# Performance work log

Measured on AMD Instinct MI355X. Metric: run time of the kernel, lower is better.

## Reference

```python
import jax, jax.numpy as jnp
import numpy as np

N, K, H = 98, 10, 4        # landmarks, neighbors/node, heads
B, CIN, HC = 1024, 256, 64 # batch, in_channels, head_channels
NEG = -9e15


def setup_inputs() -> dict:
    key = jax.random.key(0)
    ks = jax.random.split(key, 3)
    rng = np.random.default_rng(0)
    # fixed sparsity pattern: K unique neighbors per row, row-major order
    cols2d = np.stack([np.sort(rng.choice(N, K, replace=False)) for _ in range(N)])
    rows = np.repeat(np.arange(N), K)
    cols = cols2d.reshape(-1)
    x = jax.random.normal(ks[0], (B, N, CIN), jnp.float32)
    W = jax.random.normal(ks[1], (H, 2, CIN, HC), jnp.float32) * 0.05  # xavier-ish
    e = jnp.ones((H, N * K), jnp.float32)  # nn.init.constant_(e, 1)
    stdv = 1.0 / np.sqrt(HC)
    bias = jax.random.uniform(ks[2], (H, HC), jnp.float32, -stdv, stdv)
    return {"x": x, "W": W, "e": e, "bias": bias,
            "rows": jnp.asarray(rows, jnp.int32),
            "cols": jnp.asarray(cols, jnp.int32)}


def reference(x, W, e, bias, rows, cols):
    # h0/h1 for all heads at once: [2, H, B, N, HC]
    h = jnp.einsum('bnc,hscd->shbnd', x, W)
    h0, h1 = h[0], h[1]
    # masked adjacency logits per head: -9e15 everywhere, learned e at edges
    base = jnp.full((N, N), NEG, jnp.float32)
    logits = jax.vmap(lambda eh: base.at[rows, cols].set(eh))(e)  # [H,N,N]
    A = jax.nn.softmax(logits, axis=-1)  # F.softmax(adj, dim=1) on [N,N]
    diag = jnp.diagonal(A, axis1=-2, axis2=-1)  # [H,N] -> adj*M part
    A_off = A - diag[..., None] * jnp.eye(N, dtype=A.dtype)  # adj*(1-M)
    out = diag[:, None, :, None] * h0 + jnp.einsum('hij,hbjd->hbid', A_off, h1)
    out = out + bias[:, None, None, :]  # [H,B,N,HC]
    # concat heads along channel dim -> [B, N, H*HC]
    return jnp.transpose(out, (1, 2, 0, 3)).reshape(B, N, H * HC)
```

## Files before the change

kernel.cpp:

```cpp
#include <hip/hip_runtime.h>

typedef __bf16 bf16;
typedef bf16 bf16x4 __attribute__((ext_vector_type(4)));
typedef bf16 bf16x8 __attribute__((ext_vector_type(8)));
typedef float f32x4 __attribute__((ext_vector_type(4)));

#define NND 98
#define KNB 10
#define NH 4
#define CIN 256
#define HC 64
#define CROW_E 132
#define WP_BYTES 262144
#define XA_TILE (7 * 8 * 64 * 8)

__device__ __forceinline__ bf16x8 load_a8(const float* p) {
  f32x4 u = *(const f32x4*)p;
  f32x4 v = *(const f32x4*)(p + 4);
  bf16x8 a;
  a[0] = (bf16)u[0]; a[1] = (bf16)u[1]; a[2] = (bf16)u[2]; a[3] = (bf16)u[3];
  a[4] = (bf16)v[0]; a[5] = (bf16)v[1]; a[6] = (bf16)v[2]; a[7] = (bf16)v[3];
  return a;
}

__global__ __launch_bounds__(256) void prep_kernel(const float* __restrict__ W,
                                                   bf16* __restrict__ Wp,
                                                   const float* __restrict__ x,
                                                   bf16* __restrict__ xa, int B) {
  if (blockIdx.x < 64) {
    int t = blockIdx.x * 256 + threadIdx.x;
    if (t >= 8 * 8 * 4 * 64) return;
    int lane = t & 63;
    int nt = (t >> 6) & 3;
    int kt = (t >> 8) & 7;
    int hs = t >> 11;
    int n = nt * 16 + (lane & 15);
    int kb = kt * 32 + (lane >> 4) * 8;
    const float* src = W + (hs * CIN + kb) * HC + n;
    bf16x8 v;
#pragma unroll
    for (int j = 0; j < 8; ++j) v[j] = (bf16)src[j * HC];
    *(bf16x8*)(Wp + (long long)t * 8) = v;
    return;
  }
  int u = (blockIdx.x - 64) * 256 + threadIdx.x;
  int total = B * 7 * 8 * 64;
  if (u >= total) return;
  int lane = u & 63;
  int kt = (u >> 6) & 7;
  int v = u >> 9;
  int b = v / 7;
  int mt = v - b * 7;
  int row = mt * 16 + (lane & 15);
  int k0 = kt * 32 + (lane >> 4) * 8;
  bf16x8 a = {};
  if (row < NND) a = load_a8(x + ((long long)b * NND + row) * CIN + k0);
  *(bf16x8*)(xa + (long long)u * 8) = a;
}

template <bool XA>
__global__ __launch_bounds__(512, 4) void semgconv_kernel(
    const float* __restrict__ x, const bf16* __restrict__ xa,
    const float* __restrict__ e, const float* __restrict__ bias,
    const int* __restrict__ cols, const bf16* __restrict__ Wp,
    float* __restrict__ out, int nwg) {
  __shared__ __align__(16) bf16 C2[2][112 * CROW_E];
  __shared__ float w_lds[NND * KNB];
  __shared__ short cols_lds[NND * KNB];
  __shared__ float diag_lds[NND];

  const int tid = threadIdx.x;
  int n = blockIdx.x;
  int w = ((nwg & 7) == 0) ? ((n & 7) * (nwg >> 3) + (n >> 3)) : n;
  const int bp = w >> 2;
  const int h = w & 3;
  const int b0 = bp * 2;

  const int lane = tid & 63;
  const int wv = tid >> 6;
  const int wm = wv & 3;
  const int sh = wv >> 2;
  const int mt0 = wm * 2;
  const bool has1 = (mt0 + 1 < 7);

  if (tid < NND) {
    const int i = tid;
    const int* cp = cols + i * KNB;
    const float* ep = e + (h * NND + i) * KNB;
    float ev[KNB];
    int cv[KNB];
    float mx = -3.0e38f;
#pragma unroll
    for (int j = 0; j < KNB; ++j) { cv[j] = cp[j]; ev[j] = ep[j]; mx = fmaxf(mx, ev[j]); }
    float s = 0.f;
#pragma unroll
    for (int j = 0; j < KNB; ++j) { ev[j] = __expf(ev[j] - mx); s += ev[j]; }
    const float inv = 1.f / s;
    float dg = 0.f;
#pragma unroll
    for (int j = 0; j < KNB; ++j) {
      float wj = ev[j] * inv;
      if (cv[j] == i) { dg = wj; wj = 0.f; }
      w_lds[i * KNB + j] = wj;
      cols_lds[i * KNB + j] = (short)cv[j];
    }
    diag_lds[i] = dg;
  }

  f32x4 acc[2][2][4] = {};
  {
    const bf16* wpl = Wp + ((long long)((h * 2 + sh) * 32) * 64 + lane) * 8;
    if (XA) {
      const bf16* ax0 = xa + (((long long)b0 * 7 + mt0) * 8 * 64 + lane) * 8;
      const bf16* ax1 = ax0 + XA_TILE;
#pragma unroll
      for (int kt = 0; kt < 8; ++kt) {
        bf16x8 a00 = *(const bf16x8*)(ax0 + kt * 512);
        bf16x8 a10 = *(const bf16x8*)(ax1 + kt * 512);
        bf16x8 a01 = {}, a11 = {};
        if (has1) {
          a01 = *(const bf16x8*)(ax0 + 4096 + kt * 512);
          a11 = *(const bf16x8*)(ax1 + 4096 + kt * 512);
        }
        bf16x8 bfr[4];
#pragma unroll
        for (int nt = 0; nt < 4; ++nt)
          bfr[nt] = *(const bf16x8*)(wpl + (long long)((kt * 4 + nt) * 64) * 8);
#pragma unroll
        for (int nt = 0; nt < 4; ++nt) {
          acc[0][0][nt] = __builtin_amdgcn_mfma_f32_16x16x32_bf16(a00, bfr[nt], acc[0][0][nt], 0, 0, 0);
          acc[1][0][nt] = __builtin_amdgcn_mfma_f32_16x16x32_bf16(a10, bfr[nt], acc[1][0][nt], 0, 0, 0);
        }
        if (has1) {
#pragma unroll
          for (int nt = 0; nt < 4; ++nt) {
            acc[0][1][nt] = __builtin_amdgcn_mfma_f32_16x16x32_bf16(a01, bfr[nt], acc[0][1][nt], 0, 0, 0);
            acc[1][1][nt] = __builtin_amdgcn_mfma_f32_16x16x32_bf16(a11, bfr[nt], acc[1][1][nt], 0, 0, 0);
          }
        }
      }
    } else {
      const int r0 = mt0 * 16 + (lane & 15);
      const int kb = (lane >> 4) * 8;
      const bool ok0 = (r0 < NND);
#pragma unroll
      for (int kt = 0; kt < 8; ++kt) {
        bf16x8 afr[2][2];
#pragma unroll
        for (int it2 = 0; it2 < 2; ++it2) {
          const float* ap = x + ((long long)(b0 + it2) * NND + r0) * CIN + kb;
          afr[it2][0] = ok0 ? load_a8(ap + kt * 32) : bf16x8{};
          afr[it2][1] = has1 ? load_a8(ap + 16 * CIN + kt * 32) : bf16x8{};
        }
        bf16x8 bfr[4];
#pragma unroll
        for (int nt = 0; nt < 4; ++nt)
          bfr[nt] = *(const bf16x8*)(wpl + (long long)((kt * 4 + nt) * 64) * 8);
#pragma unroll
        for (int it2 = 0; it2 < 2; ++it2)
#pragma unroll
          for (int im = 0; im < 2; ++im)
            if (im == 0 || has1)
#pragma unroll
              for (int nt = 0; nt < 4; ++nt)
                acc[it2][im][nt] = __builtin_amdgcn_mfma_f32_16x16x32_bf16(
                    afr[it2][im], bfr[nt], acc[it2][im][nt], 0, 0, 0);
      }
    }
  }

  {
    const int rowb = mt0 * 16 + (lane >> 4) * 4;
    const int colb = sh * 64 + (lane & 15);
#pragma unroll
    for (int it2 = 0; it2 < 2; ++it2) {
#pragma unroll
      for (int im = 0; im < 2; ++im) {
        if (mt0 + im < 7) {
#pragma unroll
          for (int nt = 0; nt < 4; ++nt) {
            const int col = colb + nt * 16;
#pragma unroll
            for (int r = 0; r < 4; ++r)
              C2[it2][(rowb + im * 16 + r) * CROW_E + col] = (bf16)acc[it2][im][nt][r];
          }
        }
      }
    }
  }
  __syncthreads();

  {
    const int d4 = (tid & 15) * 4;
    const int ig = tid >> 4;
    f32x4 bs = *(const f32x4*)(bias + h * HC + d4);
#pragma unroll
    for (int it2 = 0; it2 < 2; ++it2) {
      const bf16* C = C2[it2];
      float* outb = out + (long long)(b0 + it2) * (NND * NH * HC) + h * HC + d4;
#pragma unroll
      for (int p = 0; p < 4; ++p) {
        const int i = p * 32 + ig;
        if (i < NND) {
          f32x4 av = bs;
          const float dg = diag_lds[i];
          bf16x4 c0 = *(const bf16x4*)(C + i * CROW_E + d4);
          av[0] += dg * (float)c0[0];
          av[1] += dg * (float)c0[1];
          av[2] += dg * (float)c0[2];
          av[3] += dg * (float)c0[3];
#pragma unroll
          for (int j = 0; j < KNB; ++j) {
            const float wj = w_lds[i * KNB + j];
            const int cj = cols_lds[i * KNB + j];
            bf16x4 c1 = *(const bf16x4*)(C + cj * CROW_E + HC + d4);
            av[0] += wj * (float)c1[0];
            av[1] += wj * (float)c1[1];
            av[2] += wj * (float)c1[2];
            av[3] += wj * (float)c1[3];
          }
          *(f32x4*)(outb + (long long)i * (NH * HC)) = av;
        }
      }
    }
  }
}

extern "C" void kernel_launch(void* const* d_in, const int* in_sizes, int n_in,
                              void* d_out, int out_size, void* d_ws, size_t ws_size,
                              hipStream_t stream) {
  const float* x    = (const float*)d_in[0];
  const float* W    = (const float*)d_in[1];
  const float* e    = (const float*)d_in[2];
  const float* bias = (const float*)d_in[3];
  const int* cols   = (const int*)d_in[5];
  float* out        = (float*)d_out;

  int B = in_sizes[0] / (NND * CIN);

  bf16* Wp = (bf16*)d_ws;
  bf16* xa = (bf16*)((char*)d_ws + WP_BYTES);
  const long long xa_bytes = (long long)B * XA_TILE * (long long)sizeof(bf16);
  const bool use_xa = (long long)ws_size >= (long long)WP_BYTES + xa_bytes;

  int xa_blocks = use_xa ? (B * 7 * 8 * 64) / 256 : 0;
  prep_kernel<<<64 + xa_blocks, 256, 0, stream>>>(W, Wp, x, xa, B);

  const int nwg = (B / 2) * NH;
  if (use_xa)
    semgconv_kernel<true><<<nwg, 512, 0, stream>>>(x, xa, e, bias, cols, Wp, out, nwg);
  else
    semgconv_kernel<false><<<nwg, 512, 0, stream>>>(x, xa, e, bias, cols, Wp, out, nwg);
}
```

Before: 240.3 us.

## Replace sparse gather aggregation with dense fp16 MFMA over precomputed adjacency

The per-row sparse gather over 10 neighbors plus diagonal term is replaced by a dense MFMA GEMM. A prep kernel builds a [112x224] fp16 adjacency matrix per head (off-diagonal weights plus diagonal weights in a second block) and packs it into MFMA fragment layout. Each workgroup stores its h0/h1 products transposed in LDS as fp16 and multiplies them against this matrix. The x-to-bf16 packing now goes through a swizzled LDS tile for coalesced access, and the non-workspace fallback path is removed. The trade is more (mostly zero) FLOPs and fp16 intermediate precision in exchange for removing scattered LDS gathers and per-block softmax work.

```diff
diff --git a/kernel.cpp b/kernel.cpp
--- a/kernel.cpp
+++ b/kernel.cpp
@@ -3,6 +3,9 @@
 typedef __bf16 bf16;
 typedef bf16 bf16x4 __attribute__((ext_vector_type(4)));
 typedef bf16 bf16x8 __attribute__((ext_vector_type(8)));
+typedef _Float16 half_t;
+typedef half_t half4 __attribute__((ext_vector_type(4)));
+typedef half_t half8 __attribute__((ext_vector_type(8)));
 typedef float f32x4 __attribute__((ext_vector_type(4)));
 
 #define NND 98
@@ -10,26 +13,25 @@
 #define NH 4
 #define CIN 256
 #define HC 64
-#define CROW_E 132
+#define KAG 224
+#define SROW 232
+#define XA_TILE (7 * 8 * 64 * 8)
+
+#define WP_OFF   0
 #define WP_BYTES 262144
-#define XA_TILE (7 * 8 * 64 * 8)
-
-__device__ __forceinline__ bf16x8 load_a8(const float* p) {
-  f32x4 u = *(const f32x4*)p;
-  f32x4 v = *(const f32x4*)(p + 4);
-  bf16x8 a;
-  a[0] = (bf16)u[0]; a[1] = (bf16)u[1]; a[2] = (bf16)u[2]; a[3] = (bf16)u[3];
-  a[4] = (bf16)v[0]; a[5] = (bf16)v[1]; a[6] = (bf16)v[2]; a[7] = (bf16)v[3];
-  return a;
-}
-
-__global__ __launch_bounds__(256) void prep_kernel(const float* __restrict__ W,
-                                                   bf16* __restrict__ Wp,
-                                                   const float* __restrict__ x,
-                                                   bf16* __restrict__ xa, int B) {
+#define G2D_OFF  (WP_OFF + WP_BYTES)
+#define G2D_BYTES (NH * 112 * KAG * 2)
+#define G2A_OFF  (G2D_OFF + G2D_BYTES)
+#define G2A_BYTES (NH * 49 * 64 * 8 * 2)
+#define XA_OFF   (G2A_OFF + G2A_BYTES)
+
+__global__ __launch_bounds__(256) void misc1_kernel(const float* __restrict__ W,
+                                                    bf16* __restrict__ Wp,
+                                                    const float* __restrict__ e,
+                                                    const int* __restrict__ cols,
+                                                    half_t* __restrict__ G2d) {
   if (blockIdx.x < 64) {
     int t = blockIdx.x * 256 + threadIdx.x;
-    if (t >= 8 * 8 * 4 * 64) return;
     int lane = t & 63;
     int nt = (t >> 6) & 3;
     int kt = (t >> 8) & 7;
@@ -43,184 +45,190 @@
     *(bf16x8*)(Wp + (long long)t * 8) = v;
     return;
   }
-  int u = (blockIdx.x - 64) * 256 + threadIdx.x;
-  int total = B * 7 * 8 * 64;
-  if (u >= total) return;
-  int lane = u & 63;
-  int kt = (u >> 6) & 7;
-  int v = u >> 9;
-  int b = v / 7;
-  int mt = v - b * 7;
-  int row = mt * 16 + (lane & 15);
-  int k0 = kt * 32 + (lane >> 4) * 8;
-  bf16x8 a = {};
-  if (row < NND) a = load_a8(x + ((long long)b * NND + row) * CIN + k0);
-  *(bf16x8*)(xa + (long long)u * 8) = a;
-}
-
-template <bool XA>
+  const int h = blockIdx.x - 64;
+  half_t* g = G2d + h * 112 * KAG;
+  for (int i = threadIdx.x; i < 112 * KAG / 2; i += 256) ((unsigned int*)g)[i] = 0u;
+  __syncthreads();
+  const int i = threadIdx.x;
+  if (i < NND) {
+    const int* cp = cols + i * KNB;
+    const float* ep = e + (h * NND + i) * KNB;
+    float ev[KNB];
+    int cv[KNB];
+    float mx = -3.0e38f;
+#pragma unroll
+    for (int j = 0; j < KNB; ++j) { cv[j] = cp[j]; ev[j] = ep[j]; mx = fmaxf(mx, ev[j]); }
+    float s = 0.f;
+#pragma unroll
+    for (int j = 0; j < KNB; ++j) { ev[j] = __expf(ev[j] - mx); s += ev[j]; }
+    const float inv = 1.f / s;
+    float dg = 0.f;
+#pragma unroll
+    for (int j = 0; j < KNB; ++j) {
+      float wj = ev[j] * inv;
+      if (cv[j] == i) { dg = wj; wj = 0.f; }
+      g[i * KAG + cv[j]] = (half_t)wj;
+    }
+    g[i * KAG + 112 + i] = (half_t)dg;
+  }
+}
+
+__global__ __launch_bounds__(256) void misc2_kernel(const half_t* __restrict__ G2d,
+                                                    half_t* __restrict__ G2a,
+                                                    const float* __restrict__ x,
+                                                    bf16* __restrict__ xa, int B) {
+  if (blockIdx.x < 49) {
+    int t = blockIdx.x * 256 + threadIdx.x;
+    int lane = t & 63;
+    int q = t >> 6;
+    int kt = q % 7;
+    int mt = (q / 7) % 7;
+    int h = q / 49;
+    int row = mt * 16 + (lane & 15);
+    int k0 = kt * 32 + (lane >> 4) * 8;
+    half8 v = *(const half8*)(G2d + (h * 112 + row) * KAG + k0);
+    *(half8*)(G2a + (long long)t * 8) = v;
+    return;
+  }
+  __shared__ __align__(16) bf16 xs[16 * 256];
+  const int b = blockIdx.x - 49;
+  const int tid = threadIdx.x;
+  const float* xb = x + (long long)b * NND * CIN;
+  for (int mt = 0; mt < 7; ++mt) {
+#pragma unroll
+    for (int it = 0; it < 4; ++it) {
+      int chunk = tid + it * 256;
+      int r = chunk >> 6;
+      int c4 = chunk & 63;
+      int g = mt * 16 + r;
+      f32x4 v = {0.f, 0.f, 0.f, 0.f};
+      if (g < NND) v = *(const f32x4*)(xb + g * CIN + c4 * 4);
+      bf16x4 bv;
+      bv[0] = (bf16)v[0]; bv[1] = (bf16)v[1]; bv[2] = (bf16)v[2]; bv[3] = (bf16)v[3];
+      int byte = (r * 512 + c4 * 8) ^ ((r & 7) << 4);
+      *(bf16x4*)((char*)xs + byte) = bv;
+    }
+    __syncthreads();
+#pragma unroll
+    for (int it = 0; it < 2; ++it) {
+      int u = tid + it * 256;
+      int kt = u >> 6;
+      int lane = u & 63;
+      int r = lane & 15;
+      int byte = (r * 512 + kt * 64 + (lane >> 4) * 16) ^ ((r & 7) << 4);
+      bf16x8 f = *(const bf16x8*)((char*)xs + byte);
+      *(bf16x8*)(xa + ((((long long)b * 7 + mt) * 8 + kt) * 64 + lane) * 8) = f;
+    }
+    __syncthreads();
+  }
+}
+
 __global__ __launch_bounds__(512, 4) void semgconv_kernel(
-    const float* __restrict__ x, const bf16* __restrict__ xa,
-    const float* __restrict__ e, const float* __restrict__ bias,
-    const int* __restrict__ cols, const bf16* __restrict__ Wp,
+    const bf16* __restrict__ xa, const half_t* __restrict__ G2a,
+    const bf16* __restrict__ Wp, const float* __restrict__ bias,
     float* __restrict__ out, int nwg) {
-  __shared__ __align__(16) bf16 C2[2][112 * CROW_E];
-  __shared__ float w_lds[NND * KNB];
-  __shared__ short cols_lds[NND * KNB];
-  __shared__ float diag_lds[NND];
+  __shared__ __align__(16) half_t S[2][64 * SROW];
 
   const int tid = threadIdx.x;
+  const int lane = tid & 63;
+  const int wv = tid >> 6;
+
   int n = blockIdx.x;
   int w = ((nwg & 7) == 0) ? ((n & 7) * (nwg >> 3) + (n >> 3)) : n;
   const int bp = w >> 2;
   const int h = w & 3;
   const int b0 = bp * 2;
 
-  const int lane = tid & 63;
-  const int wv = tid >> 6;
   const int wm = wv & 3;
   const int sh = wv >> 2;
   const int mt0 = wm * 2;
   const bool has1 = (mt0 + 1 < 7);
 
-  if (tid < NND) {
-    const int i = tid;
-    const int* cp = cols + i * KNB;
-    const float* ep = e + (h * NND + i) * KNB;
-    float ev[KNB];
-    int cv[KNB];
-    float mx = -3.0e38f;
-#pragma unroll
-    for (int j = 0; j < KNB; ++j) { cv[j] = cp[j]; ev[j] = ep[j]; mx = fmaxf(mx, ev[j]); }
-    float s = 0.f;
-#pragma unroll
-    for (int j = 0; j < KNB; ++j) { ev[j] = __expf(ev[j] - mx); s += ev[j]; }
-    const float inv = 1.f / s;
-    float dg = 0.f;
-#pragma unroll
-    for (int j = 0; j < KNB; ++j) {
-      float wj = ev[j] * inv;
-      if (cv[j] == i) { dg = wj; wj = 0.f; }
-      w_lds[i * KNB + j] = wj;
-      cols_lds[i * KNB + j] = (short)cv[j];
-    }
-    diag_lds[i] = dg;
-  }
-
   f32x4 acc[2][2][4] = {};
   {
     const bf16* wpl = Wp + ((long long)((h * 2 + sh) * 32) * 64 + lane) * 8;
-    if (XA) {
-      const bf16* ax0 = xa + (((long long)b0 * 7 + mt0) * 8 * 64 + lane) * 8;
-      const bf16* ax1 = ax0 + XA_TILE;
-#pragma unroll
-      for (int kt = 0; kt < 8; ++kt) {
-        bf16x8 a00 = *(const bf16x8*)(ax0 + kt * 512);
-        bf16x8 a10 = *(const bf16x8*)(ax1 + kt * 512);
-        bf16x8 a01 = {}, a11 = {};
-        if (has1) {
-          a01 = *(const bf16x8*)(ax0 + 4096 + kt * 512);
-          a11 = *(const bf16x8*)(ax1 + 4096 + kt * 512);
+    const bf16* ax0 = xa + (((long long)b0 * 7 + mt0) * 8 * 64 + lane) * 8;
+    const bf16* ax1 = ax0 + XA_TILE;
+#pragma unroll
+    for (int kt = 0; kt < 8; ++kt) {
+      bf16x8 a00 = *(const bf16x8*)(ax0 + kt * 512);
+      bf16x8 a10 = *(const bf16x8*)(ax1 + kt * 512);
+      bf16x8 a01 = {}, a11 = {};
+      if (has1) {
+        a01 = *(const bf16x8*)(ax0 + 4096 + kt * 512);
+        a11 = *(const bf16x8*)(ax1 + 4096 + kt * 512);
+      }
+      bf16x8 bfr[4];
+#pragma unroll
+      for (int nt = 0; nt < 4; ++nt)
+        bfr[nt] = *(const bf16x8*)(wpl + (long long)((kt * 4 + nt) * 64) * 8);
+#pragma unroll
+      for (int nt = 0; nt < 4; ++nt) {
+        acc[0][0][nt] = __builtin_amdgcn_mfma_f32_16x16x32_bf16(a00, bfr[nt], acc[0][0][nt], 0, 0, 0);
+        acc[1][0][nt] = __builtin_amdgcn_mfma_f32_16x16x32_bf16(a10, bfr[nt], acc[1][0][nt], 0, 0, 0);
+      }
+      if (has1) {
+#pragma unroll
+        for (int nt = 0; nt < 4; ++nt) {
+          acc[0][1][nt] = __builtin_amdgcn_mfma_f32_16x16x32_bf16(a01, bfr[nt], acc[0][1][nt], 0, 0, 0);
+          acc[1][1][nt] = __builtin_amdgcn_mfma_f32_16x16x32_bf16(a11, bfr[nt], acc[1][1][nt], 0, 0, 0);
         }
-        bf16x8 bfr[4];
-#pragma unroll
-        for (int nt = 0; nt < 4; ++nt)
-          bfr[nt] = *(const bf16x8*)(wpl + (long long)((kt * 4 + nt) * 64) * 8);
-#pragma unroll
-        for (int nt = 0; nt < 4; ++nt) {
-          acc[0][0][nt] = __builtin_amdgcn_mfma_f32_16x16x32_bf16(a00, bfr[nt], acc[0][0][nt], 0, 0, 0);
-          acc[1][0][nt] = __builtin_amdgcn_mfma_f32_16x16x32_bf16(a10, bfr[nt], acc[1][0][nt], 0, 0, 0);
-        }
-        if (has1) {
+      }
+    }
+  }
+
+  {
+    const int jb = (sh ? 0 : 112) + (lane >> 4) * 4;
+    const int cb = lane & 15;
+#pragma unroll
+    for (int it2 = 0; it2 < 2; ++it2) {
+#pragma unroll
+      for (int im = 0; im < 2; ++im) {
+        if (mt0 + im < 7) {
+          const int j0 = jb + (mt0 + im) * 16;
 #pragma unroll
           for (int nt = 0; nt < 4; ++nt) {
-            acc[0][1][nt] = __builtin_amdgcn_mfma_f32_16x16x32_bf16(a01, bfr[nt], acc[0][1][nt], 0, 0, 0);
-            acc[1][1][nt] = __builtin_amdgcn_mfma_f32_16x16x32_bf16(a11, bfr[nt], acc[1][1][nt], 0, 0, 0);
+            half4 hv;
+            hv[0] = (half_t)acc[it2][im][nt][0];
+            hv[1] = (half_t)acc[it2][im][nt][1];
+            hv[2] = (half_t)acc[it2][im][nt][2];
+            hv[3] = (half_t)acc[it2][im][nt][3];
+            *(half4*)(&S[it2][(nt * 16 + cb) * SROW + j0]) = hv;
           }
         }
       }
-    } else {
-      const int r0 = mt0 * 16 + (lane & 15);
-      const int kb = (lane >> 4) * 8;
-      const bool ok0 = (r0 < NND);
-#pragma unroll
-      for (int kt = 0; kt < 8; ++kt) {
-        bf16x8 afr[2][2];
-#pragma unroll
-        for (int it2 = 0; it2 < 2; ++it2) {
-          const float* ap = x + ((long long)(b0 + it2) * NND + r0) * CIN + kb;
-          afr[it2][0] = ok0 ? load_a8(ap + kt * 32) : bf16x8{};
-          afr[it2][1] = has1 ? load_a8(ap + 16 * CIN + kt * 32) : bf16x8{};
-        }
-        bf16x8 bfr[4];
-#pragma unroll
-        for (int nt = 0; nt < 4; ++nt)
-          bfr[nt] = *(const bf16x8*)(wpl + (long long)((kt * 4 + nt) * 64) * 8);
-#pragma unroll
-        for (int it2 = 0; it2 < 2; ++it2)
-#pragma unroll
-          for (int im = 0; im < 2; ++im)
-            if (im == 0 || has1)
-#pragma unroll
-              for (int nt = 0; nt < 4; ++nt)
-                acc[it2][im][nt] = __builtin_amdgcn_mfma_f32_16x16x32_bf16(
-                    afr[it2][im], bfr[nt], acc[it2][im][nt], 0, 0, 0);
-      }
-    }
-  }
-
-  {
-    const int rowb = mt0 * 16 + (lane >> 4) * 4;
-    const int colb = sh * 64 + (lane & 15);
-#pragma unroll
-    for (int it2 = 0; it2 < 2; ++it2) {
-#pragma unroll
-      for (int im = 0; im < 2; ++im) {
-        if (mt0 + im < 7) {
-#pragma unroll
-          for (int nt = 0; nt < 4; ++nt) {
-            const int col = colb + nt * 16;
-#pragma unroll
-            for (int r = 0; r < 4; ++r)
-              C2[it2][(rowb + im * 16 + r) * CROW_E + col] = (bf16)acc[it2][im][nt][r];
-          }
-        }
-      }
     }
   }
   __syncthreads();
 
-  {
-    const int d4 = (tid & 15) * 4;
-    const int ig = tid >> 4;
-    f32x4 bs = *(const f32x4*)(bias + h * HC + d4);
-#pragma unroll
-    for (int it2 = 0; it2 < 2; ++it2) {
-      const bf16* C = C2[it2];
-      float* outb = out + (long long)(b0 + it2) * (NND * NH * HC) + h * HC + d4;
-#pragma unroll
-      for (int p = 0; p < 4; ++p) {
-        const int i = p * 32 + ig;
-        if (i < NND) {
-          f32x4 av = bs;
-          const float dg = diag_lds[i];
-          bf16x4 c0 = *(const bf16x4*)(C + i * CROW_E + d4);
-          av[0] += dg * (float)c0[0];
-          av[1] += dg * (float)c0[1];
-          av[2] += dg * (float)c0[2];
-          av[3] += dg * (float)c0[3];
-#pragma unroll
-          for (int j = 0; j < KNB; ++j) {
-            const float wj = w_lds[i * KNB + j];
-            const int cj = cols_lds[i * KNB + j];
-            bf16x4 c1 = *(const bf16x4*)(C + cj * CROW_E + HC + d4);
-            av[0] += wj * (float)c1[0];
-            av[1] += wj * (float)c1[1];
-            av[2] += wj * (float)c1[2];
-            av[3] += wj * (float)c1[3];
-          }
-          *(f32x4*)(outb + (long long)i * (NH * HC)) = av;
-        }
+  const int it2 = wv & 1;
+  const int nt2 = wv >> 1;
+  f32x4 a2[7] = {};
+  {
+    const half_t* g2l = G2a + ((long long)h * 49 * 64 + lane) * 8;
+    const half_t* sl = &S[it2][(nt2 * 16 + (lane & 15)) * SROW + (lane >> 4) * 8];
+#pragma unroll
+    for (int kt = 0; kt < 7; ++kt) {
+      half8 bfr = *(const half8*)(sl + kt * 32);
+#pragma unroll
+      for (int mt = 0; mt < 7; ++mt) {
+        half8 afr = *(const half8*)(g2l + (long long)(mt * 7 + kt) * 64 * 8);
+        a2[mt] = __builtin_amdgcn_mfma_f32_16x16x32_f16(afr, bfr, a2[mt], 0, 0, 0);
+      }
+    }
+  }
+
+  {
+    const int col = nt2 * 16 + (lane & 15);
+    const float bs = bias[h * HC + col];
+    const int r0 = (lane >> 4) * 4;
+    float* ob = out + (long long)(b0 + it2) * NND * (NH * HC) + h * HC + col;
+#pragma unroll
+    for (int mt = 0; mt < 7; ++mt) {
+#pragma unroll
+      for (int r = 0; r < 4; ++r) {
+        const int row = mt * 16 + r0 + r;
+        if (row < NND) ob[(long long)row * (NH * HC)] = a2[mt][r] + bs;
       }
     }
   }
@@ -238,17 +246,14 @@
 
   int B = in_sizes[0] / (NND * CIN);
 
-  bf16* Wp = (bf16*)d_ws;
-  bf16* xa = (bf16*)((char*)d_ws + WP_BYTES);
-  const long long xa_bytes = (long long)B * XA_TILE * (long long)sizeof(bf16);
-  const bool use_xa = (long long)ws_size >= (long long)WP_BYTES + xa_bytes;
-
-  int xa_blocks = use_xa ? (B * 7 * 8 * 64) / 256 : 0;
-  prep_kernel<<<64 + xa_blocks, 256, 0, stream>>>(W, Wp, x, xa, B);
+  bf16* Wp    = (bf16*)((char*)d_ws + WP_OFF);
+  half_t* G2d = (half_t*)((char*)d_ws + G2D_OFF);
+  half_t* G2a = (half_t*)((char*)d_ws + G2A_OFF);
+  bf16* xa    = (bf16*)((char*)d_ws + XA_OFF);
+
+  misc1_kernel<<<68, 256, 0, stream>>>(W, Wp, e, cols, G2d);
+  misc2_kernel<<<49 + B, 256, 0, stream>>>(G2d, G2a, x, xa, B);
 
   const int nwg = (B / 2) * NH;
-  if (use_xa)
-    semgconv_kernel<true><<<nwg, 512, 0, stream>>>(x, xa, e, bias, cols, Wp, out, nwg);
-  else
-    semgconv_kernel<false><<<nwg, 512, 0, stream>>>(x, xa, e, bias, cols, Wp, out, nwg);
-}
+  semgconv_kernel<<<nwg, 512, 0, stream>>>(xa, G2a, Wp, bias, out, nwg);
+}
```

Result: slower. 258.3 us (+7.5%).
